# Optimization experiments

Measured on AMD Instinct MI355X. Metric: run time of the kernel, lower is better.

Reference implementation:

```python
import jax, jax.numpy as jnp
import numpy as np

DIM = 1536
NHEADS = 12
HDIM = DIM // NHEADS  # 128
EPS = 1e-6
LOCAL_ATTN_SIZE = 3
SINK_SIZE = 1
MAX_ATTN = 32760 if LOCAL_ATTN_SIZE == -1 else LOCAL_ATTN_SIZE * 1560  # 4680


def _rms(x, g):
    # WanRMSNorm over last dim
    return x * jax.lax.rsqrt(jnp.mean(x * x, axis=-1, keepdims=True) + EPS) * g


def _rope(x, f, h, w, fr, fi, start_frame):
    # x: [b, s, n, d] with s == f*h*w; fr/fi: [1024, d//2] real/imag of complex rotations
    b, s, n, d = x.shape
    c = d // 2
    c0 = c - 2 * (c // 3)
    c1 = c // 3
    fc = jax.lax.complex(fr, fi)  # [1024, c]
    xr = x.reshape(b, s, n, c, 2)
    xc = jax.lax.complex(xr[..., 0], xr[..., 1])  # [b, s, n, c]
    ff = fc[start_frame:start_frame + f, :c0]      # [f, c0]
    fh = fc[:h, c0:c0 + c1]                        # [h, c1]
    fw = fc[:w, c0 + c1:c0 + 2 * c1]               # [w, c1]
    freqs_i = jnp.concatenate([
        jnp.broadcast_to(ff[:, None, None, :], (f, h, w, c0)),
        jnp.broadcast_to(fh[None, :, None, :], (f, h, w, c1)),
        jnp.broadcast_to(fw[None, None, :, :], (f, h, w, c1)),
    ], axis=-1).reshape(1, s, 1, c)
    y = xc * freqs_i
    return jnp.stack([y.real, y.imag], axis=-1).reshape(b, s, n, d)


def _attn(q, k, v):
    # plain SDPA (decode path of the module uses no mask on the gathered window)
    scale = 1.0 / np.sqrt(q.shape[-1]).astype(np.float32)
    logits = jnp.einsum('bqnd,bknd->bnqk', q, k) * scale
    p = jax.nn.softmax(logits, axis=-1)
    return jnp.einsum('bnqk,bknd->bqnd', p, v)


def _forward(x, cache_k, cache_v, freqs_real, freqs_imag,
             wq, bq, wk, bk, wv, bv, wo, bo, gq, gk,
             f_frames, height, width, current_start, global_end_index, local_end_index):
    b, s, _ = x.shape
    n, d = NHEADS, HDIM
    frame_seqlen = height * width
    start_frame = current_start // frame_seqlen

    q = _rms(x @ wq + bq, gq).reshape(b, s, n, d)
    k = _rms(x @ wk + bk, gk).reshape(b, s, n, d)
    v = (x @ wv + bv).reshape(b, s, n, d)

    rq = _rope(q, f_frames, height, width, freqs_real, freqs_imag, start_frame)
    rk = _rope(k, f_frames, height, width, freqs_real, freqs_imag, start_frame)

    current_end = current_start + s
    sink_tokens = SINK_SIZE * frame_seqlen
    kv_size = cache_k.shape[1]
    is_recompute = (current_end <= global_end_index) and (current_start > 0)

    kc, vc = cache_k, cache_v
    if LOCAL_ATTN_SIZE != -1 and current_end > global_end_index and s + local_end_index > kv_size:
        # evict oldest non-sink tokens, roll the rest toward the sink region
        num_evicted = s + local_end_index - kv_size
        num_rolled = local_end_index - num_evicted - sink_tokens
        src = slice(sink_tokens + num_evicted, sink_tokens + num_evicted + num_rolled)
        kc = kc.at[:, sink_tokens:sink_tokens + num_rolled].set(jax.lax.stop_gradient(cache_k[:, src]))
        vc = vc.at[:, sink_tokens:sink_tokens + num_rolled].set(jax.lax.stop_gradient(cache_v[:, src]))
        new_local_end = local_end_index + current_end - global_end_index - num_evicted
    else:
        new_local_end = local_end_index + current_end - global_end_index
    local_start = new_local_end - s
    write_start = max(local_start, sink_tokens) if is_recompute else local_start
    off = max(0, write_start - local_start)
    wl = max(0, new_local_end - write_start)
    if wl > 0:
        kc = kc.at[:, write_start:new_local_end].set(rk[:, off:off + wl])
        vc = vc.at[:, write_start:new_local_end].set(v[:, off:off + wl])

    if sink_tokens > 0:
        budget = MAX_ATTN - sink_tokens
        if budget > 0:
            lo = max(sink_tokens, new_local_end - budget)
            kcat = jnp.concatenate([kc[:, :sink_tokens], kc[:, lo:new_local_end]], axis=1)
            vcat = jnp.concatenate([vc[:, :sink_tokens], vc[:, lo:new_local_end]], axis=1)
        else:
            kcat, vcat = kc[:, :sink_tokens], vc[:, :sink_tokens]
        o = _attn(rq, kcat, vcat)
    else:
        ws = max(0, new_local_end - MAX_ATTN)
        o = _attn(rq, kc[:, ws:new_local_end], vc[:, ws:new_local_end])

    return o.reshape(b, s, DIM) @ wo + bo


def setup_inputs() -> dict:
    key = jax.random.key(0)
    ks = jax.random.split(key, 12)
    B, S, CACHE = 1, 1560, 4680
    sc = 0.02
    # RoPE tables as unit-magnitude complex rotations
    ang = jax.random.uniform(ks[0], (1024, HDIM // 2), jnp.float32, 0.0, 2.0 * np.pi)
    return {
        'x': jax.random.normal(ks[1], (B, S, DIM), jnp.float32),
        'cache_k': jax.random.normal(ks[2], (B, CACHE, NHEADS, HDIM), jnp.float32),
        'cache_v': jax.random.normal(ks[3], (B, CACHE, NHEADS, HDIM), jnp.float32),
        'freqs_real': jnp.cos(ang),
        'freqs_imag': jnp.sin(ang),
        'wq': jax.random.normal(ks[4], (DIM, DIM), jnp.float32) * sc,
        'bq': jnp.zeros((DIM,), jnp.float32),
        'wk': jax.random.normal(ks[5], (DIM, DIM), jnp.float32) * sc,
        'bk': jnp.zeros((DIM,), jnp.float32),
        'wv': jax.random.normal(ks[6], (DIM, DIM), jnp.float32) * sc,
        'bv': jnp.zeros((DIM,), jnp.float32),
        'wo': jax.random.normal(ks[7], (DIM, DIM), jnp.float32) * sc,
        'bo': jnp.zeros((DIM,), jnp.float32),
        'gq': jnp.ones((DIM,), jnp.float32),
        'gk': jnp.ones((DIM,), jnp.float32),
        'f_frames': 1,
        'height': 30,
        'width': 52,
        'current_start': 4680,
        'global_end_index': 4680,
        'local_end_index': 4680,
    }


def reference(x, cache_k, cache_v, freqs_real, freqs_imag,
              wq, bq, wk, bk, wv, bv, wo, bo, gq, gk,
              f_frames, height, width, current_start, global_end_index, local_end_index):
    return _forward(x, cache_k, cache_v, freqs_real, freqs_imag,
                    wq, bq, wk, bk, wv, bv, wo, bo, gq, gk,
                    f_frames, height, width, current_start, global_end_index, local_end_index)
```

## Files before the change

kernel.cpp:

```cpp
#include <hip/hip_runtime.h>
#include <cstdint>
#include <cstddef>

typedef unsigned int  u32;
typedef unsigned short u16;
typedef short s16x8 __attribute__((ext_vector_type(8)));
typedef float f32x4 __attribute__((ext_vector_type(4)));

#define DIM     1536
#define NH      12
#define HD      128
#define SEQ     1560
#define MPAD    1664
#define NKV     4680
#define NKPAD   4736
#define ROLL0   3120
#define NQK     4608
#define START_FRAME 3
#define NEGINF  -3.0e4f
#define NSPLIT  4
#define SPLITKC 1216

__device__ __forceinline__ u16 f2bf(float f){
  u32 u = __builtin_bit_cast(u32, f);
  u32 r = (u + 0x7fffu + ((u >> 16) & 1u)) >> 16;
  return (u16)r;
}

__global__ void k_pre(const float* __restrict__ x, u16* __restrict__ xp,
                      u16* __restrict__ Kc, u16* __restrict__ VT,
                      u16* __restrict__ Qr, u16* __restrict__ Opad,
                      float* __restrict__ sumsq){
  int b = blockIdx.x;
  if (b < 244){
    int i = b * 256 + threadIdx.x;
    uint4 z = make_uint4(0u, 0u, 0u, 0u);
    if (i < 10752){
      int h = i / 896, r = i % 896;
      ((uint4*)(Kc + ((size_t)h * NKPAD + NKV) * 128))[r] = z;
    } else if (i < 21504){
      int j = i - 10752; int row = j / 7, c = j % 7;
      ((uint4*)(VT + (size_t)row * NKPAD + NKV))[c] = z;
    } else if (i < 41472){
      int j = i - 21504; int h = j / 1664, r = j % 1664;
      ((uint4*)(Qr + ((size_t)h * MPAD + SEQ) * 128))[r] = z;
    } else if (i < 61440){
      int r = i - 41472;
      ((uint4*)(Opad + (size_t)SEQ * DIM))[r] = z;
    } else if (i < 62272){
      ((uint4*)sumsq)[i - 61440] = z;
    }
  } else {
    int i = (b - 244) * 256 + threadIdx.x;
    const int n_src = SEQ * DIM / 8;
    u16 o[8] = {0,0,0,0,0,0,0,0};
    if (i < n_src){
      float4 a = ((const float4*)x)[2*i];
      float4 c = ((const float4*)x)[2*i + 1];
      o[0]=f2bf(a.x); o[1]=f2bf(a.y); o[2]=f2bf(a.z); o[3]=f2bf(a.w);
      o[4]=f2bf(c.x); o[5]=f2bf(c.y); o[6]=f2bf(c.z); o[7]=f2bf(c.w);
    }
    uint4 v = make_uint4((u32)o[0]|((u32)o[1]<<16), (u32)o[2]|((u32)o[3]<<16),
                         (u32)o[4]|((u32)o[5]<<16), (u32)o[6]|((u32)o[7]<<16));
    ((uint4*)xp)[i] = v;
  }
}

__global__ void k_transpose_w(const float* __restrict__ wq, const float* __restrict__ wk,
                              const float* __restrict__ wv, const float* __restrict__ wo,
                              u16* __restrict__ WTqkv, u16* __restrict__ WTo){
  __shared__ u32 tile[64][65];
  int z = blockIdx.z;
  const float* w = (z==0)?wq:(z==1)?wk:(z==2)?wv:wo;
  u16* dst = (z < 3) ? (WTqkv + (size_t)z * DIM * DIM) : WTo;
  int r0 = blockIdx.x * 64, c0 = blockIdx.y * 64;
  int t = threadIdx.x;
  int rr = t >> 4, cg = t & 15;
#pragma unroll
  for (int i = 0; i < 4; i++){
    int r = rr + i * 16;
    float4 v = *(const float4*)(w + (size_t)(r0 + r) * DIM + c0 + cg * 4);
    tile[r][cg*4+0] = f2bf(v.x); tile[r][cg*4+1] = f2bf(v.y);
    tile[r][cg*4+2] = f2bf(v.z); tile[r][cg*4+3] = f2bf(v.w);
  }
  __syncthreads();
  int c = t >> 2, rg = t & 3;
  u32 wds[8];
#pragma unroll
  for (int j = 0; j < 8; j++)
    wds[j] = (tile[rg*16 + 2*j][c] & 0xffffu) | (tile[rg*16 + 2*j + 1][c] << 16);
  u16* q = dst + (size_t)(c0 + c) * DIM + r0 + rg * 16;
  *(uint4*)q       = make_uint4(wds[0], wds[1], wds[2], wds[3]);
  *(uint4*)(q + 8) = make_uint4(wds[4], wds[5], wds[6], wds[7]);
}

#define LDK 40
__global__ __launch_bounds__(256) void k_gemm_qkv(
    const u16* __restrict__ A, const u16* __restrict__ B,
    const float* __restrict__ biasq, const float* __restrict__ biask, const float* __restrict__ biasv,
    float* __restrict__ Y, float* __restrict__ sumsq){
  __shared__ u16 As[128*LDK];
  __shared__ u16 Bs[128*LDK];
  int m0 = blockIdx.y * 128, n0 = blockIdx.x * 128;
  int t = threadIdx.x, w = t >> 6, lane = t & 63, quad = lane >> 4, lc = lane & 15;
  int wm = w & 1, wn = w >> 1;
  int sr = t >> 1, sh = (t & 1) * 16;
  f32x4 acc[4][4] = {};
  for (int kt = 0; kt < DIM/32; kt++){
    int k0 = kt * 32;
    __syncthreads();
    {
      const uint4* ga = (const uint4*)(A + (size_t)(m0 + sr) * DIM + k0 + sh);
      uint4 a0 = ga[0], a1 = ga[1];
      const uint4* gb = (const uint4*)(B + (size_t)(n0 + sr) * DIM + k0 + sh);
      uint4 b0 = gb[0], b1 = gb[1];
      *(uint4*)(As + sr * LDK + sh)     = a0;
      *(uint4*)(As + sr * LDK + sh + 8) = a1;
      *(uint4*)(Bs + sr * LDK + sh)     = b0;
      *(uint4*)(Bs + sr * LDK + sh + 8) = b1;
    }
    __syncthreads();
    s16x8 af[4], bf[4];
#pragma unroll
    for (int mt = 0; mt < 4; mt++) af[mt] = *(const s16x8*)(As + (wm*64 + mt*16 + lc) * LDK + quad * 8);
#pragma unroll
    for (int nt = 0; nt < 4; nt++) bf[nt] = *(const s16x8*)(Bs + (wn*64 + nt*16 + lc) * LDK + quad * 8);
#pragma unroll
    for (int mt = 0; mt < 4; mt++)
#pragma unroll
      for (int nt = 0; nt < 4; nt++)
        acc[mt][nt] = __builtin_amdgcn_mfma_f32_16x16x32_bf16(af[mt], bf[nt], acc[mt][nt], 0, 0, 0);
  }
  const float* bias; int cbase; int which;
  if (n0 < DIM)        { bias = biasq; cbase = 0;     which = 0; }
  else if (n0 < 2*DIM) { bias = biask; cbase = DIM;   which = 1; }
  else                 { bias = biasv; cbase = 2*DIM; which = 2; }
  float bvals[4];
#pragma unroll
  for (int nt = 0; nt < 4; nt++) bvals[nt] = bias[n0 - cbase + wn*64 + nt*16 + lc];
#pragma unroll
  for (int mt = 0; mt < 4; mt++){
    int row0 = m0 + wm*64 + mt*16 + quad*4;
    float ss[4] = {0.f, 0.f, 0.f, 0.f};
#pragma unroll
    for (int nt = 0; nt < 4; nt++){
      int col = n0 + wn*64 + nt*16 + lc;
#pragma unroll
      for (int r = 0; r < 4; r++){
        float y = acc[mt][nt][r] + bvals[nt];
        Y[(size_t)(row0 + r) * NQK + col] = y;
        ss[r] += y * y;
      }
    }
    if (which < 2){
      float* dst = sumsq + (which ? MPAD : 0);
#pragma unroll
      for (int r = 0; r < 4; r++){
        float v = ss[r];
        v += __shfl_xor(v, 1); v += __shfl_xor(v, 2); v += __shfl_xor(v, 4); v += __shfl_xor(v, 8);
        if (lc == 0) atomicAdd(&dst[row0 + r], v);
      }
    }
  }
}

__global__ void k_rope_qk(const float* __restrict__ Y, const float* __restrict__ sumsq,
                          const float* __restrict__ gq, const float* __restrict__ gk,
                          const float* __restrict__ fre, const float* __restrict__ fim,
                          u16* __restrict__ Qr, u16* __restrict__ Kc){
  int pos = blockIdx.x;
  int t = threadIdx.x;
  float scq = rsqrtf(sumsq[pos]        * (1.0f/1536.0f) + 1e-6f);
  float sck = rsqrtf(sumsq[MPAD + pos] * (1.0f/1536.0f) + 1e-6f);
  int hrow = pos / 52, wrow = pos % 52;
#pragma unroll
  for (int i = 0; i < 3; i++){
    int p = t + i * 256;
    int head = p >> 6, j = p & 63;
    int frow = (j < 22) ? START_FRAME : ((j < 43) ? hrow : wrow);
    float cr = fre[frow * 64 + j], ci = fim[frow * 64 + j];
    int d0 = head * 128 + 2 * j;
    float2 yq = *(const float2*)(Y + (size_t)pos * NQK + d0);
    float qa = yq.x * scq * gq[d0];
    float qb = yq.y * scq * gq[d0 + 1];
    u32 oq = (u32)f2bf(qa * cr - qb * ci) | ((u32)f2bf(qa * ci + qb * cr) << 16);
    *(u32*)(Qr + (size_t)(head * MPAD + pos) * 128 + 2 * j) = oq;
    float2 yk = *(const float2*)(Y + (size_t)pos * NQK + DIM + d0);
    float ka = yk.x * sck * gk[d0];
    float kb = yk.y * sck * gk[d0 + 1];
    u32 ok = (u32)f2bf(ka * cr - kb * ci) | ((u32)f2bf(ka * ci + kb * cr) << 16);
    *(u32*)(Kc + (size_t)(head * NKPAD + ROLL0 + pos) * 128 + 2 * j) = ok;
  }
}

__global__ void k_copy_cache_k(const float* __restrict__ ck, u16* __restrict__ Kc){
  int p = blockIdx.x;
  int src = (p < SEQ) ? p : p + SEQ;
  int t = threadIdx.x;
  int h = t >> 4, d = (t & 15) * 8;
  const float* s = ck + (size_t)src * DIM + t * 8;
  float4 a = ((const float4*)s)[0], b = ((const float4*)s)[1];
  uint4 v = make_uint4((u32)f2bf(a.x)|((u32)f2bf(a.y)<<16), (u32)f2bf(a.z)|((u32)f2bf(a.w)<<16),
                       (u32)f2bf(b.x)|((u32)f2bf(b.y)<<16), (u32)f2bf(b.z)|((u32)f2bf(b.w)<<16));
  *(uint4*)(Kc + (size_t)(h * NKPAD + p) * 128 + d) = v;
}

__global__ void k_tv_cache(const float* __restrict__ cv, u16* __restrict__ VT){
  __shared__ u32 tile[64][65];
  int p0 = blockIdx.x * 64, hd0 = blockIdx.y * 64;
  int t = threadIdx.x;
  int pr = t >> 4, cg = t & 15;
#pragma unroll
  for (int i = 0; i < 4; i++){
    int p = p0 + pr + i * 16;
    if (p < ROLL0){
      int src = (p < SEQ) ? p : p + SEQ;
      float4 v = *(const float4*)(cv + (size_t)src * DIM + hd0 + cg * 4);
      tile[pr + i*16][cg*4+0] = f2bf(v.x); tile[pr + i*16][cg*4+1] = f2bf(v.y);
      tile[pr + i*16][cg*4+2] = f2bf(v.z); tile[pr + i*16][cg*4+3] = f2bf(v.w);
    }
  }
  __syncthreads();
  int hd = t >> 2, pg = t & 3;
  int pbase = p0 + pg * 16;
  if (pbase < ROLL0){
    u32 wds[8];
#pragma unroll
    for (int j = 0; j < 8; j++)
      wds[j] = (tile[pg*16 + 2*j][hd] & 0xffffu) | (tile[pg*16 + 2*j + 1][hd] << 16);
    u16* q = VT + (size_t)(hd0 + hd) * NKPAD + pbase;
    *(uint4*)q       = make_uint4(wds[0], wds[1], wds[2], wds[3]);
    *(uint4*)(q + 8) = make_uint4(wds[4], wds[5], wds[6], wds[7]);
  }
}

__global__ void k_tv_new(const float* __restrict__ Y, u16* __restrict__ VT){
  __shared__ u32 tile[64][65];
  int p0 = blockIdx.x * 64, hd0 = blockIdx.y * 64;
  int t = threadIdx.x;
  int pr = t >> 4, cg = t & 15;
#pragma unroll
  for (int i = 0; i < 4; i++){
    int p = p0 + pr + i * 16;
    if (p < SEQ){
      float4 v = *(const float4*)(Y + (size_t)p * NQK + 2*DIM + hd0 + cg * 4);
      tile[pr + i*16][cg*4+0] = f2bf(v.x); tile[pr + i*16][cg*4+1] = f2bf(v.y);
      tile[pr + i*16][cg*4+2] = f2bf(v.z); tile[pr + i*16][cg*4+3] = f2bf(v.w);
    }
  }
  __syncthreads();
  int hd = t >> 2, pg = t & 3;
  int pbase = p0 + pg * 16;
  u32 wds[8];
#pragma unroll
  for (int j = 0; j < 8; j++)
    wds[j] = (tile[pg*16 + 2*j][hd] & 0xffffu) | (tile[pg*16 + 2*j + 1][hd] << 16);
  u16* q = VT + (size_t)(hd0 + hd) * NKPAD + ROLL0 + pbase;
  if (pbase + 8  <= SEQ) *(uint4*)q       = make_uint4(wds[0], wds[1], wds[2], wds[3]);
  if (pbase + 16 <= SEQ) *(uint4*)(q + 8) = make_uint4(wds[4], wds[5], wds[6], wds[7]);
}

#define DEFER_THR 8.0f
__global__ __launch_bounds__(512, 4) void k_attn(const u16* __restrict__ Qr, const u16* __restrict__ Kc,
                                                 const u16* __restrict__ VT,
                                                 float* __restrict__ Opart, float* __restrict__ ml){
  __shared__ u16 Ks[64 * 128];
  __shared__ u16 Vs[128 * 64];
  int h = blockIdx.y, qb = blockIdx.x, sp = blockIdx.z;
  int t = threadIdx.x, w = t >> 6, lane = t & 63, quad = lane >> 4, lc = lane & 15;
  int qbase = qb * 128 + w * 16;
  const u16* Qbase = Qr + (size_t)(h * MPAD + qbase + lc) * 128;
  s16x8 qf[4];
#pragma unroll
  for (int kk = 0; kk < 4; kk++) qf[kk] = *(const s16x8*)(Qbase + kk * 32 + quad * 8);
  f32x4 oacc[8] = {};
  float m_ = NEGINF;
  float l_ = 0.f;
  const float scale = 0.08838834764831845f;
  const u16* Kh = Kc + (size_t)h * NKPAD * 128;
  const u16* Vh = VT + (size_t)h * 128 * NKPAD;
  int kr0 = t >> 4,          kg0 = (t & 15) * 8;
  int kr1 = (t + 512) >> 4,  kg1 = ((t + 512) & 15) * 8;
  int vd0 = t >> 3,          vp0 = (t & 7) * 8;
  int vd1 = (t + 512) >> 3,  vp1 = ((t + 512) & 7) * 8;
  int ksw0 = kr0 * 128 + (kg0 ^ ((kr0 & 7) << 3));
  int ksw1 = kr1 * 128 + (kg1 ^ ((kr1 & 7) << 3));
  int vsw0 = vd0 * 64  + (vp0 ^ ((vd0 & 7) << 3));
  int vsw1 = vd1 * 64  + (vp1 ^ ((vd1 & 7) << 3));
  int xork = (lc & 7) << 3;
  int aa = (lc + ((quad & 1) << 5)) << 2;
  int ab = aa + 64;
  int hi = quad >> 1;

  int kc0 = sp * SPLITKC;
  int kc1 = (sp == NSPLIT-1) ? NKPAD : kc0 + SPLITKC;
  uint4 kp0, kp1, vq0, vq1;
  {
    int kc = kc0;
    kp0 = *(const uint4*)(Kh + (size_t)(kc + kr0) * 128 + kg0);
    kp1 = *(const uint4*)(Kh + (size_t)(kc + kr1) * 128 + kg1);
    vq0 = *(const uint4*)(Vh + (size_t)vd0 * NKPAD + kc + vp0);
    vq1 = *(const uint4*)(Vh + (size_t)vd1 * NKPAD + kc + vp1);
  }
  for (int kc = kc0; kc < kc1; kc += 64){
    __syncthreads();
    *(uint4*)(Ks + ksw0) = kp0;
    *(uint4*)(Ks + ksw1) = kp1;
    *(uint4*)(Vs + vsw0) = vq0;
    *(uint4*)(Vs + vsw1) = vq1;
    __syncthreads();
    if (kc + 64 < kc1){
      int kn = kc + 64;
      kp0 = *(const uint4*)(Kh + (size_t)(kn + kr0) * 128 + kg0);
      kp1 = *(const uint4*)(Kh + (size_t)(kn + kr1) * 128 + kg1);
      vq0 = *(const uint4*)(Vh + (size_t)vd0 * NKPAD + kn + vp0);
      vq1 = *(const uint4*)(Vh + (size_t)vd1 * NKPAD + kn + vp1);
    }
    float s[4][4];
    __builtin_amdgcn_s_setprio(1);
#pragma unroll
    for (int nt = 0; nt < 4; nt++){
      f32x4 acc = {};
      int p = nt * 16 + lc;
#pragma unroll
      for (int kk = 0; kk < 4; kk++){
        s16x8 kf = *(const s16x8*)(Ks + p * 128 + (((kk * 4 + quad) * 8) ^ xork));
        acc = __builtin_amdgcn_mfma_f32_16x16x32_bf16(kf, qf[kk], acc, 0, 0, 0);
      }
#pragma unroll
      for (int r = 0; r < 4; r++) s[nt][r] = acc[r] * scale;
    }
    __builtin_amdgcn_s_setprio(0);
    if (kc + 64 > NKV){
#pragma unroll
      for (int nt = 0; nt < 4; nt++){
        int keyb = kc + nt * 16 + quad * 4;
#pragma unroll
        for (int r = 0; r < 4; r++) if (keyb + r >= NKV) s[nt][r] = NEGINF;
      }
    }
    float mx = fmaxf(fmaxf(s[0][0], s[0][1]), fmaxf(s[0][2], s[0][3]));
#pragma unroll
    for (int nt = 1; nt < 4; nt++)
      mx = fmaxf(mx, fmaxf(fmaxf(s[nt][0], s[nt][1]), fmaxf(s[nt][2], s[nt][3])));
    mx = fmaxf(mx, __shfl_xor(mx, 16));
    mx = fmaxf(mx, __shfl_xor(mx, 32));
    if (__any(mx > m_ + DEFER_THR)){
      float mnew = fmaxf(m_, mx);
      float alpha = __expf(m_ - mnew);
      m_ = mnew; l_ *= alpha;
      float alr[4];
#pragma unroll
      for (int r = 0; r < 4; r++) alr[r] = __shfl(alpha, quad * 4 + r);
#pragma unroll
      for (int dt = 0; dt < 8; dt++){
        f32x4 oo = oacc[dt];
#pragma unroll
        for (int r = 0; r < 4; r++) oo[r] *= alr[r];
        oacc[dt] = oo;
      }
    }
#pragma unroll
    for (int nt = 0; nt < 4; nt++)
#pragma unroll
      for (int r = 0; r < 4; r++) s[nt][r] = __expf(s[nt][r] - m_);
    float sum = (s[0][0] + s[0][1]) + (s[0][2] + s[0][3]);
#pragma unroll
    for (int nt = 1; nt < 4; nt++)
      sum += (s[nt][0] + s[nt][1]) + (s[nt][2] + s[nt][3]);
    sum += __shfl_xor(sum, 16);
    sum += __shfl_xor(sum, 32);
    l_ += sum;
    u32 w01[4], w23[4];
#pragma unroll
    for (int nt = 0; nt < 4; nt++){
      w01[nt] = (u32)f2bf(s[nt][0]) | ((u32)f2bf(s[nt][1]) << 16);
      w23[nt] = (u32)f2bf(s[nt][2]) | ((u32)f2bf(s[nt][3]) << 16);
    }
    u32 x0, x1;
    uint4 A0, A1;
    x0 = (u32)__builtin_amdgcn_ds_bpermute(aa, (int)w01[0]);
    x1 = (u32)__builtin_amdgcn_ds_bpermute(aa, (int)w01[1]);
    A0.x = hi ? x1 : x0;
    x0 = (u32)__builtin_amdgcn_ds_bpermute(aa, (int)w23[0]);
    x1 = (u32)__builtin_amdgcn_ds_bpermute(aa, (int)w23[1]);
    A0.y = hi ? x1 : x0;
    x0 = (u32)__builtin_amdgcn_ds_bpermute(ab, (int)w01[0]);
    x1 = (u32)__builtin_amdgcn_ds_bpermute(ab, (int)w01[1]);
    A0.z = hi ? x1 : x0;
    x0 = (u32)__builtin_amdgcn_ds_bpermute(ab, (int)w23[0]);
    x1 = (u32)__builtin_amdgcn_ds_bpermute(ab, (int)w23[1]);
    A0.w = hi ? x1 : x0;
    x0 = (u32)__builtin_amdgcn_ds_bpermute(aa, (int)w01[2]);
    x1 = (u32)__builtin_amdgcn_ds_bpermute(aa, (int)w01[3]);
    A1.x = hi ? x1 : x0;
    x0 = (u32)__builtin_amdgcn_ds_bpermute(aa, (int)w23[2]);
    x1 = (u32)__builtin_amdgcn_ds_bpermute(aa, (int)w23[3]);
    A1.y = hi ? x1 : x0;
    x0 = (u32)__builtin_amdgcn_ds_bpermute(ab, (int)w01[2]);
    x1 = (u32)__builtin_amdgcn_ds_bpermute(ab, (int)w01[3]);
    A1.z = hi ? x1 : x0;
    x0 = (u32)__builtin_amdgcn_ds_bpermute(ab, (int)w23[2]);
    x1 = (u32)__builtin_amdgcn_ds_bpermute(ab, (int)w23[3]);
    A1.w = hi ? x1 : x0;
    s16x8 a0 = __builtin_bit_cast(s16x8, A0);
    s16x8 a1 = __builtin_bit_cast(s16x8, A1);
    __builtin_amdgcn_s_setprio(1);
#pragma unroll
    for (int dt = 0; dt < 8; dt++){
      int d = dt * 16 + lc;
      s16x8 v0 = *(const s16x8*)(Vs + d * 64 + ((quad * 8) ^ xork));
      s16x8 v1 = *(const s16x8*)(Vs + d * 64 + ((32 + quad * 8) ^ xork));
      oacc[dt] = __builtin_amdgcn_mfma_f32_16x16x32_bf16(a0, v0, oacc[dt], 0, 0, 0);
      oacc[dt] = __builtin_amdgcn_mfma_f32_16x16x32_bf16(a1, v1, oacc[dt], 0, 0, 0);
    }
    __builtin_amdgcn_s_setprio(0);
  }
  float mr[4], lr[4];
#pragma unroll
  for (int r = 0; r < 4; r++){
    mr[r] = __shfl(m_, quad * 4 + r);
    lr[r] = __shfl(l_, quad * 4 + r);
  }
  float* Ob = Opart + ((size_t)(sp * NH + h) * SEQ) * 128;
  float* mlb = ml + ((size_t)(sp * NH + h) * SEQ) * 2;
#pragma unroll
  for (int dt = 0; dt < 8; dt++)
#pragma unroll
    for (int r = 0; r < 4; r++){
      int row = qbase + quad * 4 + r;
      if (row < SEQ) Ob[(size_t)row * 128 + dt * 16 + lc] = oacc[dt][r];
    }
  if (lc == 0){
#pragma unroll
    for (int r = 0; r < 4; r++){
      int row = qbase + quad * 4 + r;
      if (row < SEQ){
        mlb[row * 2 + 0] = mr[r];
        mlb[row * 2 + 1] = lr[r];
      }
    }
  }
}

__global__ void k_attn_cmb(const float* __restrict__ Opart, const float* __restrict__ ml,
                           u16* __restrict__ Og){
  int row = blockIdx.x, h = blockIdx.y, d = threadIdx.x;
  float m[NSPLIT], l[NSPLIT];
  float M = NEGINF;
#pragma unroll
  for (int s = 0; s < NSPLIT; s++){
    m[s] = ml[((size_t)(s * NH + h) * SEQ + row) * 2 + 0];
    l[s] = ml[((size_t)(s * NH + h) * SEQ + row) * 2 + 1];
    M = fmaxf(M, m[s]);
  }
  float L = 0.f, o = 0.f;
#pragma unroll
  for (int s = 0; s < NSPLIT; s++){
    float wgt = __expf(m[s] - M);
    L += wgt * l[s];
    o += wgt * Opart[((size_t)(s * NH + h) * SEQ + row) * 128 + d];
  }
  Og[(size_t)row * DIM + h * 128 + d] = f2bf(o / L);
}

__global__ __launch_bounds__(256) void k_gemm_out(const u16* __restrict__ A, const u16* __restrict__ B,
                                                  const float* __restrict__ bo, float* __restrict__ out){
  __shared__ u16 As[128*LDK];
  __shared__ u16 Bs[128*LDK];
  int m0 = blockIdx.y * 128, n0 = blockIdx.x * 128;
  int t = threadIdx.x, w = t >> 6, lane = t & 63, quad = lane >> 4, lc = lane & 15;
  int wm = w & 1, wn = w >> 1;
  int sr = t >> 1, sh = (t & 1) * 16;
  f32x4 acc[4][4] = {};
  for (int kt = 0; kt < DIM/32; kt++){
    int k0 = kt * 32;
    __syncthreads();
    {
      const uint4* ga = (const uint4*)(A + (size_t)(m0 + sr) * DIM + k0 + sh);
      uint4 a0 = ga[0], a1 = ga[1];
      const uint4* gb = (const uint4*)(B + (size_t)(n0 + sr) * DIM + k0 + sh);
      uint4 b0 = gb[0], b1 = gb[1];
      *(uint4*)(As + sr * LDK + sh)     = a0;
      *(uint4*)(As + sr * LDK + sh + 8) = a1;
      *(uint4*)(Bs + sr * LDK + sh)     = b0;
      *(uint4*)(Bs + sr * LDK + sh + 8) = b1;
    }
    __syncthreads();
    s16x8 af[4], bf[4];
#pragma unroll
    for (int mt = 0; mt < 4; mt++) af[mt] = *(const s16x8*)(As + (wm*64 + mt*16 + lc) * LDK + quad * 8);
#pragma unroll
    for (int nt = 0; nt < 4; nt++) bf[nt] = *(const s16x8*)(Bs + (wn*64 + nt*16 + lc) * LDK + quad * 8);
#pragma unroll
    for (int mt = 0; mt < 4; mt++)
#pragma unroll
      for (int nt = 0; nt < 4; nt++)
        acc[mt][nt] = __builtin_amdgcn_mfma_f32_16x16x32_bf16(af[mt], bf[nt], acc[mt][nt], 0, 0, 0);
  }
  float bvals[4];
#pragma unroll
  for (int nt = 0; nt < 4; nt++) bvals[nt] = bo[n0 + wn*64 + nt*16 + lc];
#pragma unroll
  for (int mt = 0; mt < 4; mt++){
    int row0 = m0 + wm*64 + mt*16 + quad*4;
#pragma unroll
    for (int nt = 0; nt < 4; nt++){
      int col = n0 + wn*64 + nt*16 + lc;
#pragma unroll
      for (int r = 0; r < 4; r++){
        int row = row0 + r;
        if (row < SEQ) out[(size_t)row * DIM + col] = acc[mt][nt][r] + bvals[nt];
      }
    }
  }
}

extern "C" void kernel_launch(void* const* d_in, const int* in_sizes, int n_in,
                              void* d_out, int out_size, void* d_ws, size_t ws_size,
                              hipStream_t stream){
  const float* x   = (const float*)d_in[0];
  const float* ck  = (const float*)d_in[1];
  const float* cv  = (const float*)d_in[2];
  const float* fre = (const float*)d_in[3];
  const float* fim = (const float*)d_in[4];
  const float* wq  = (const float*)d_in[5];
  const float* bq  = (const float*)d_in[6];
  const float* wk  = (const float*)d_in[7];
  const float* bk  = (const float*)d_in[8];
  const float* wv  = (const float*)d_in[9];
  const float* bv  = (const float*)d_in[10];
  const float* wo  = (const float*)d_in[11];
  const float* bo  = (const float*)d_in[12];
  const float* gq  = (const float*)d_in[13];
  const float* gk  = (const float*)d_in[14];

  char* ws = (char*)d_ws;
  size_t off = 0;
  u16*   xpad  = (u16*)(ws + off);  off += (size_t)MPAD * DIM * 2;
  u16*   WTqkv = (u16*)(ws + off);  off += (size_t)3 * DIM * DIM * 2;
  float* Y     = (float*)(ws + off); off += (size_t)MPAD * NQK * 4;
  u16*   WTo   = (u16*)(ws + off);  off += (size_t)DIM * DIM * 2;
  float* sumsq = (float*)(ws + off); off += (size_t)2 * MPAD * 4;
  u16*   Qr    = (u16*)(ws + off);  off += (size_t)NH * MPAD * 128 * 2;
  u16*   Kc    = (u16*)(ws + off);  off += (size_t)NH * NKPAD * 128 * 2;
  u16*   VT    = (u16*)(ws + off);  off += (size_t)NH * 128 * NKPAD * 2;
  u16*   Opad  = (u16*)(ws + off);  off += (size_t)MPAD * DIM * 2;
  if (off > ws_size) return;
  float* Opart = (float*)ws;
  float* ml    = (float*)(ws + (size_t)NSPLIT * NH * SEQ * 128 * 4);

  k_pre         <<<dim3(1492), 256, 0, stream>>>(x, xpad, Kc, VT, Qr, Opad, sumsq);
  k_transpose_w <<<dim3(24, 24, 4), 256, 0, stream>>>(wq, wk, wv, wo, WTqkv, WTo);
  k_gemm_qkv    <<<dim3(NQK/128, MPAD/128), 256, 0, stream>>>(xpad, WTqkv, bq, bk, bv, Y, sumsq);
  k_rope_qk     <<<dim3(SEQ), 256, 0, stream>>>(Y, sumsq, gq, gk, fre, fim, Qr, Kc);
  k_copy_cache_k<<<dim3(ROLL0), 192, 0, stream>>>(ck, Kc);
  k_tv_cache    <<<dim3(49, 24), 256, 0, stream>>>(cv, VT);
  k_tv_new      <<<dim3(25, 24), 256, 0, stream>>>(Y, VT);
  k_attn        <<<dim3(MPAD/128, NH, NSPLIT), 512, 0, stream>>>(Qr, Kc, VT, Opart, ml);
  k_attn_cmb    <<<dim3(SEQ, NH), 128, 0, stream>>>(Opart, ml, Opad);
  k_gemm_out    <<<dim3(DIM/128, MPAD/128), 256, 0, stream>>>(Opad, WTo, bo, (float*)d_out);
}
```

Measured before the change: 377.3 us.

## Fuse cache conversions into pre kernel, write V transposed from GEMM, prefetch GEMM tiles

Folds the K-cache copy and V-cache transpose into the k_pre launch as extra block ranges. The QKV GEMM epilogue now writes V directly as transposed bf16 into VT, which removes the separate k_tv_new kernel and the fp32 V store to Y. Both GEMMs gain register prefetching of the next K-tile's global loads, overlapping them with the MFMA work. This cuts three launches and some round trips through memory, at the cost of a larger, more branchy k_pre and strided uint2 stores in the GEMM epilogue.

Measured after the change: 357.4 us. 5.3% less time.

```diff
diff --git a/kernel.cpp b/kernel.cpp
--- a/kernel.cpp
+++ b/kernel.cpp
@@ -30,10 +30,12 @@
 __global__ void k_pre(const float* __restrict__ x, u16* __restrict__ xp,
                       u16* __restrict__ Kc, u16* __restrict__ VT,
                       u16* __restrict__ Qr, u16* __restrict__ Opad,
-                      float* __restrict__ sumsq){
-  int b = blockIdx.x;
+                      float* __restrict__ sumsq,
+                      const float* __restrict__ ck, const float* __restrict__ cv){
+  __shared__ u32 tile[64][65];
+  int b = blockIdx.x, t = threadIdx.x;
   if (b < 244){
-    int i = b * 256 + threadIdx.x;
+    int i = b * 256 + t;
     uint4 z = make_uint4(0u, 0u, 0u, 0u);
     if (i < 10752){
       int h = i / 896, r = i % 896;
@@ -50,8 +52,8 @@
     } else if (i < 62272){
       ((uint4*)sumsq)[i - 61440] = z;
     }
-  } else {
-    int i = (b - 244) * 256 + threadIdx.x;
+  } else if (b < 1492){
+    int i = (b - 244) * 256 + t;
     const int n_src = SEQ * DIM / 8;
     u16 o[8] = {0,0,0,0,0,0,0,0};
     if (i < n_src){
@@ -63,6 +65,42 @@
     uint4 v = make_uint4((u32)o[0]|((u32)o[1]<<16), (u32)o[2]|((u32)o[3]<<16),
                          (u32)o[4]|((u32)o[5]<<16), (u32)o[6]|((u32)o[7]<<16));
     ((uint4*)xp)[i] = v;
+  } else if (b < 3832){
+    int i = (b - 1492) * 256 + t;
+    int p = i / 192, j = i - p * 192;
+    int src = (p < SEQ) ? p : p + SEQ;
+    int h = j >> 4, d = (j & 15) * 8;
+    const float* s = ck + (size_t)src * DIM + j * 8;
+    float4 a = ((const float4*)s)[0], bb = ((const float4*)s)[1];
+    uint4 v = make_uint4((u32)f2bf(a.x)|((u32)f2bf(a.y)<<16), (u32)f2bf(a.z)|((u32)f2bf(a.w)<<16),
+                         (u32)f2bf(bb.x)|((u32)f2bf(bb.y)<<16), (u32)f2bf(bb.z)|((u32)f2bf(bb.w)<<16));
+    *(uint4*)(Kc + (size_t)(h * NKPAD + p) * 128 + d) = v;
+  } else {
+    int idx = b - 3832;
+    int p0 = (idx % 49) * 64, hd0 = (idx / 49) * 64;
+    int pr = t >> 4, cg = t & 15;
+#pragma unroll
+    for (int i = 0; i < 4; i++){
+      int p = p0 + pr + i * 16;
+      if (p < ROLL0){
+        int src = (p < SEQ) ? p : p + SEQ;
+        float4 v = *(const float4*)(cv + (size_t)src * DIM + hd0 + cg * 4);
+        tile[pr + i*16][cg*4+0] = f2bf(v.x); tile[pr + i*16][cg*4+1] = f2bf(v.y);
+        tile[pr + i*16][cg*4+2] = f2bf(v.z); tile[pr + i*16][cg*4+3] = f2bf(v.w);
+      }
+    }
+    __syncthreads();
+    int hd = t >> 2, pg = t & 3;
+    int pbase = p0 + pg * 16;
+    if (pbase < ROLL0){
+      u32 wds[8];
+#pragma unroll
+      for (int j = 0; j < 8; j++)
+        wds[j] = (tile[pg*16 + 2*j][hd] & 0xffffu) | (tile[pg*16 + 2*j + 1][hd] << 16);
+      u16* q = VT + (size_t)(hd0 + hd) * NKPAD + pbase;
+      *(uint4*)q       = make_uint4(wds[0], wds[1], wds[2], wds[3]);
+      *(uint4*)(q + 8) = make_uint4(wds[4], wds[5], wds[6], wds[7]);
+    }
   }
 }
 
@@ -98,7 +136,7 @@
 __global__ __launch_bounds__(256) void k_gemm_qkv(
     const u16* __restrict__ A, const u16* __restrict__ B,
     const float* __restrict__ biasq, const float* __restrict__ biask, const float* __restrict__ biasv,
-    float* __restrict__ Y, float* __restrict__ sumsq){
+    float* __restrict__ Y, float* __restrict__ sumsq, u16* __restrict__ VT){
   __shared__ u16 As[128*LDK];
   __shared__ u16 Bs[128*LDK];
   int m0 = blockIdx.y * 128, n0 = blockIdx.x * 128;
@@ -106,20 +144,25 @@
   int wm = w & 1, wn = w >> 1;
   int sr = t >> 1, sh = (t & 1) * 16;
   f32x4 acc[4][4] = {};
+  uint4 pa0, pa1, pb0, pb1;
+  {
+    const uint4* ga = (const uint4*)(A + (size_t)(m0 + sr) * DIM + sh);
+    const uint4* gb = (const uint4*)(B + (size_t)(n0 + sr) * DIM + sh);
+    pa0 = ga[0]; pa1 = ga[1]; pb0 = gb[0]; pb1 = gb[1];
+  }
   for (int kt = 0; kt < DIM/32; kt++){
-    int k0 = kt * 32;
-    __syncthreads();
-    {
+    __syncthreads();
+    *(uint4*)(As + sr * LDK + sh)     = pa0;
+    *(uint4*)(As + sr * LDK + sh + 8) = pa1;
+    *(uint4*)(Bs + sr * LDK + sh)     = pb0;
+    *(uint4*)(Bs + sr * LDK + sh + 8) = pb1;
+    __syncthreads();
+    if (kt + 1 < DIM/32){
+      int k0 = (kt + 1) * 32;
       const uint4* ga = (const uint4*)(A + (size_t)(m0 + sr) * DIM + k0 + sh);
-      uint4 a0 = ga[0], a1 = ga[1];
       const uint4* gb = (const uint4*)(B + (size_t)(n0 + sr) * DIM + k0 + sh);
-      uint4 b0 = gb[0], b1 = gb[1];
-      *(uint4*)(As + sr * LDK + sh)     = a0;
-      *(uint4*)(As + sr * LDK + sh + 8) = a1;
-      *(uint4*)(Bs + sr * LDK + sh)     = b0;
-      *(uint4*)(Bs + sr * LDK + sh + 8) = b1;
-    }
-    __syncthreads();
+      pa0 = ga[0]; pa1 = ga[1]; pb0 = gb[0]; pb1 = gb[1];
+    }
     s16x8 af[4], bf[4];
 #pragma unroll
     for (int mt = 0; mt < 4; mt++) af[mt] = *(const s16x8*)(As + (wm*64 + mt*16 + lc) * LDK + quad * 8);
@@ -138,21 +181,35 @@
   float bvals[4];
 #pragma unroll
   for (int nt = 0; nt < 4; nt++) bvals[nt] = bias[n0 - cbase + wn*64 + nt*16 + lc];
-#pragma unroll
-  for (int mt = 0; mt < 4; mt++){
-    int row0 = m0 + wm*64 + mt*16 + quad*4;
-    float ss[4] = {0.f, 0.f, 0.f, 0.f};
-#pragma unroll
-    for (int nt = 0; nt < 4; nt++){
-      int col = n0 + wn*64 + nt*16 + lc;
-#pragma unroll
-      for (int r = 0; r < 4; r++){
-        float y = acc[mt][nt][r] + bvals[nt];
-        Y[(size_t)(row0 + r) * NQK + col] = y;
-        ss[r] += y * y;
-      }
-    }
-    if (which < 2){
+  if (which == 2){
+#pragma unroll
+    for (int mt = 0; mt < 4; mt++){
+      int row0 = m0 + wm*64 + mt*16 + quad*4;
+      if (row0 < SEQ){
+#pragma unroll
+        for (int nt = 0; nt < 4; nt++){
+          int hd = (n0 - 2*DIM) + wn*64 + nt*16 + lc;
+          u32 lo = (u32)f2bf(acc[mt][nt][0] + bvals[nt]) | ((u32)f2bf(acc[mt][nt][1] + bvals[nt]) << 16);
+          u32 hi = (u32)f2bf(acc[mt][nt][2] + bvals[nt]) | ((u32)f2bf(acc[mt][nt][3] + bvals[nt]) << 16);
+          *(uint2*)(VT + (size_t)hd * NKPAD + ROLL0 + row0) = make_uint2(lo, hi);
+        }
+      }
+    }
+  } else {
+#pragma unroll
+    for (int mt = 0; mt < 4; mt++){
+      int row0 = m0 + wm*64 + mt*16 + quad*4;
+      float ss[4] = {0.f, 0.f, 0.f, 0.f};
+#pragma unroll
+      for (int nt = 0; nt < 4; nt++){
+        int col = n0 + wn*64 + nt*16 + lc;
+#pragma unroll
+        for (int r = 0; r < 4; r++){
+          float y = acc[mt][nt][r] + bvals[nt];
+          Y[(size_t)(row0 + r) * NQK + col] = y;
+          ss[r] += y * y;
+        }
+      }
       float* dst = sumsq + (which ? MPAD : 0);
 #pragma unroll
       for (int r = 0; r < 4; r++){
@@ -191,73 +248,6 @@
     u32 ok = (u32)f2bf(ka * cr - kb * ci) | ((u32)f2bf(ka * ci + kb * cr) << 16);
     *(u32*)(Kc + (size_t)(head * NKPAD + ROLL0 + pos) * 128 + 2 * j) = ok;
   }
-}
-
-__global__ void k_copy_cache_k(const float* __restrict__ ck, u16* __restrict__ Kc){
-  int p = blockIdx.x;
-  int src = (p < SEQ) ? p : p + SEQ;
-  int t = threadIdx.x;
-  int h = t >> 4, d = (t & 15) * 8;
-  const float* s = ck + (size_t)src * DIM + t * 8;
-  float4 a = ((const float4*)s)[0], b = ((const float4*)s)[1];
-  uint4 v = make_uint4((u32)f2bf(a.x)|((u32)f2bf(a.y)<<16), (u32)f2bf(a.z)|((u32)f2bf(a.w)<<16),
-                       (u32)f2bf(b.x)|((u32)f2bf(b.y)<<16), (u32)f2bf(b.z)|((u32)f2bf(b.w)<<16));
-  *(uint4*)(Kc + (size_t)(h * NKPAD + p) * 128 + d) = v;
-}
-
-__global__ void k_tv_cache(const float* __restrict__ cv, u16* __restrict__ VT){
-  __shared__ u32 tile[64][65];
-  int p0 = blockIdx.x * 64, hd0 = blockIdx.y * 64;
-  int t = threadIdx.x;
-  int pr = t >> 4, cg = t & 15;
-#pragma unroll
-  for (int i = 0; i < 4; i++){
-    int p = p0 + pr + i * 16;
-    if (p < ROLL0){
-      int src = (p < SEQ) ? p : p + SEQ;
-      float4 v = *(const float4*)(cv + (size_t)src * DIM + hd0 + cg * 4);
-      tile[pr + i*16][cg*4+0] = f2bf(v.x); tile[pr + i*16][cg*4+1] = f2bf(v.y);
-      tile[pr + i*16][cg*4+2] = f2bf(v.z); tile[pr + i*16][cg*4+3] = f2bf(v.w);
-    }
-  }
-  __syncthreads();
-  int hd = t >> 2, pg = t & 3;
-  int pbase = p0 + pg * 16;
-  if (pbase < ROLL0){
-    u32 wds[8];
-#pragma unroll
-    for (int j = 0; j < 8; j++)
-      wds[j] = (tile[pg*16 + 2*j][hd] & 0xffffu) | (tile[pg*16 + 2*j + 1][hd] << 16);
-    u16* q = VT + (size_t)(hd0 + hd) * NKPAD + pbase;
-    *(uint4*)q       = make_uint4(wds[0], wds[1], wds[2], wds[3]);
-    *(uint4*)(q + 8) = make_uint4(wds[4], wds[5], wds[6], wds[7]);
-  }
-}
-
-__global__ void k_tv_new(const float* __restrict__ Y, u16* __restrict__ VT){
-  __shared__ u32 tile[64][65];
-  int p0 = blockIdx.x * 64, hd0 = blockIdx.y * 64;
-  int t = threadIdx.x;
-  int pr = t >> 4, cg = t & 15;
-#pragma unroll
-  for (int i = 0; i < 4; i++){
-    int p = p0 + pr + i * 16;
-    if (p < SEQ){
-      float4 v = *(const float4*)(Y + (size_t)p * NQK + 2*DIM + hd0 + cg * 4);
-      tile[pr + i*16][cg*4+0] = f2bf(v.x); tile[pr + i*16][cg*4+1] = f2bf(v.y);
-      tile[pr + i*16][cg*4+2] = f2bf(v.z); tile[pr + i*16][cg*4+3] = f2bf(v.w);
-    }
-  }
-  __syncthreads();
-  int hd = t >> 2, pg = t & 3;
-  int pbase = p0 + pg * 16;
-  u32 wds[8];
-#pragma unroll
-  for (int j = 0; j < 8; j++)
-    wds[j] = (tile[pg*16 + 2*j][hd] & 0xffffu) | (tile[pg*16 + 2*j + 1][hd] << 16);
-  u16* q = VT + (size_t)(hd0 + hd) * NKPAD + ROLL0 + pbase;
-  if (pbase + 8  <= SEQ) *(uint4*)q       = make_uint4(wds[0], wds[1], wds[2], wds[3]);
-  if (pbase + 16 <= SEQ) *(uint4*)(q + 8) = make_uint4(wds[4], wds[5], wds[6], wds[7]);
 }
 
 #define DEFER_THR 8.0f
@@ -473,20 +463,25 @@
   int wm = w & 1, wn = w >> 1;
   int sr = t >> 1, sh = (t & 1) * 16;
   f32x4 acc[4][4] = {};
+  uint4 pa0, pa1, pb0, pb1;
+  {
+    const uint4* ga = (const uint4*)(A + (size_t)(m0 + sr) * DIM + sh);
+    const uint4* gb = (const uint4*)(B + (size_t)(n0 + sr) * DIM + sh);
+    pa0 = ga[0]; pa1 = ga[1]; pb0 = gb[0]; pb1 = gb[1];
+  }
   for (int kt = 0; kt < DIM/32; kt++){
-    int k0 = kt * 32;
-    __syncthreads();
-    {
+    __syncthreads();
+    *(uint4*)(As + sr * LDK + sh)     = pa0;
+    *(uint4*)(As + sr * LDK + sh + 8) = pa1;
+    *(uint4*)(Bs + sr * LDK + sh)     = pb0;
+    *(uint4*)(Bs + sr * LDK + sh + 8) = pb1;
+    __syncthreads();
+    if (kt + 1 < DIM/32){
+      int k0 = (kt + 1) * 32;
       const uint4* ga = (const uint4*)(A + (size_t)(m0 + sr) * DIM + k0 + sh);
-      uint4 a0 = ga[0], a1 = ga[1];
       const uint4* gb = (const uint4*)(B + (size_t)(n0 + sr) * DIM + k0 + sh);
-      uint4 b0 = gb[0], b1 = gb[1];
-      *(uint4*)(As + sr * LDK + sh)     = a0;
-      *(uint4*)(As + sr * LDK + sh + 8) = a1;
-      *(uint4*)(Bs + sr * LDK + sh)     = b0;
-      *(uint4*)(Bs + sr * LDK + sh + 8) = b1;
-    }
-    __syncthreads();
+      pa0 = ga[0]; pa1 = ga[1]; pb0 = gb[0]; pb1 = gb[1];
+    }
     s16x8 af[4], bf[4];
 #pragma unroll
     for (int mt = 0; mt < 4; mt++) af[mt] = *(const s16x8*)(As + (wm*64 + mt*16 + lc) * LDK + quad * 8);
@@ -550,13 +545,10 @@
   float* Opart = (float*)ws;
   float* ml    = (float*)(ws + (size_t)NSPLIT * NH * SEQ * 128 * 4);
 
-  k_pre         <<<dim3(1492), 256, 0, stream>>>(x, xpad, Kc, VT, Qr, Opad, sumsq);
+  k_pre         <<<dim3(5008), 256, 0, stream>>>(x, xpad, Kc, VT, Qr, Opad, sumsq, ck, cv);
   k_transpose_w <<<dim3(24, 24, 4), 256, 0, stream>>>(wq, wk, wv, wo, WTqkv, WTo);
-  k_gemm_qkv    <<<dim3(NQK/128, MPAD/128), 256, 0, stream>>>(xpad, WTqkv, bq, bk, bv, Y, sumsq);
+  k_gemm_qkv    <<<dim3(NQK/128, MPAD/128), 256, 0, stream>>>(xpad, WTqkv, bq, bk, bv, Y, sumsq, VT);
   k_rope_qk     <<<dim3(SEQ), 256, 0, stream>>>(Y, sumsq, gq, gk, fre, fim, Qr, Kc);
-  k_copy_cache_k<<<dim3(ROLL0), 192, 0, stream>>>(ck, Kc);
-  k_tv_cache    <<<dim3(49, 24), 256, 0, stream>>>(cv, VT);
-  k_tv_new      <<<dim3(25, 24), 256, 0, stream>>>(Y, VT);
   k_attn        <<<dim3(MPAD/128, NH, NSPLIT), 512, 0, stream>>>(Qr, Kc, VT, Opart, ml);
   k_attn_cmb    <<<dim3(SEQ, NH), 128, 0, stream>>>(Opart, ml, Opad);
   k_gemm_out    <<<dim3(DIM/128, MPAD/128), 256, 0, stream>>>(Opad, WTo, bo, (float*)d_out);
```
